# Performance work log

Measured on AMD Instinct MI355X. Metric: run time of the kernel, lower is better.

## Reference

```python
import jax, jax.numpy as jnp
import numpy as np

HEADS = 8
DIM_HEAD = 64
SCALE = DIM_HEAD ** -0.5


def setup_inputs() -> dict:
    key = jax.random.key(0)
    ks = jax.random.split(key, 7)
    B, N, M, D, INNER = 2, 4096, 4096, 1024, HEADS * DIM_HEAD
    x = jax.random.normal(ks[0], (B, N, D), dtype=jnp.float32)
    context = jax.random.normal(ks[1], (B, M, D), dtype=jnp.float32)
    Wq = jax.random.normal(ks[2], (D, INNER), dtype=jnp.float32) * 0.02
    Wk = jax.random.normal(ks[3], (D, INNER), dtype=jnp.float32) * 0.02
    Wv = jax.random.normal(ks[4], (D, INNER), dtype=jnp.float32) * 0.02
    Wo = jax.random.normal(ks[5], (INNER, D), dtype=jnp.float32) * 0.02
    bo = jnp.zeros((D,), dtype=jnp.float32)
    return {"x": x, "context": context, "Wq": Wq, "Wk": Wk, "Wv": Wv, "Wo": Wo, "bo": bo}


def reference(x, context, Wq, Wk, Wv, Wo, bo):
    B, N, _ = x.shape
    M = context.shape[1]
    # projections (no bias, as in to_q/to_k/to_v)
    q = (x @ Wq).reshape(B, N, HEADS, DIM_HEAD)        # b n h d
    k = (context @ Wk).reshape(B, M, HEADS, DIM_HEAD)  # b m h d
    v = (context @ Wv).reshape(B, M, HEADS, DIM_HEAD)
    # scaled dot-product attention (the chunk loop in the original is math-equivalent)
    scores = jnp.einsum('bnhd,bmhd->bhnm', q, k) * SCALE
    attn = jax.nn.softmax(scores, axis=-1)
    out = jnp.einsum('bhnm,bmhd->bnhd', attn, v).reshape(B, N, HEADS * DIM_HEAD)
    # to_out: Linear with bias (dropout p=0.0 -> identity)
    return out @ Wo + bo
```

## Files before the change

### kernel.cpp

```cpp
#include <hip/hip_runtime.h>
#include <hip/hip_bf16.h>

typedef short bf16x8 __attribute__((ext_vector_type(8)));
typedef float f32x4 __attribute__((ext_vector_type(4)));
typedef float f32x16 __attribute__((ext_vector_type(16)));

#define MFMA16(a, b, c) __builtin_amdgcn_mfma_f32_16x16x32_bf16((a), (b), (c), 0, 0, 0)
#define MFMA32(a, b, c) __builtin_amdgcn_mfma_f32_32x32x16_bf16((a), (b), (c), 0, 0, 0)

#if __has_builtin(__builtin_amdgcn_exp2f)
#define EXP2(x) __builtin_amdgcn_exp2f(x)
#else
#define EXP2(x) __expf((x) * 0.6931471805599453f)
#endif

__device__ __forceinline__ ushort f2bf(float f) {
  union { float f; unsigned u; } x; x.f = f;
  unsigned u = x.u;
  return (ushort)((u + 0x7fffu + ((u >> 16) & 1u)) >> 16);
}

__device__ __forceinline__ unsigned cvtpk(float a, float b) {
  unsigned r;
  asm("v_cvt_pk_bf16_f32 %0, %1, %2" : "=v"(r) : "v"(a), "v"(b));
  return r;
}

__device__ __forceinline__ void plswap(unsigned& a, unsigned& b) {
  asm volatile("v_permlane32_swap_b32 %0, %1" : "+v"(a), "+v"(b));
}

__device__ __forceinline__ float bfbits2f(unsigned hw) {
  union { unsigned u; float f; } x; x.u = hw << 16; return x.f;
}

__device__ __forceinline__ void gl2lds16(const ushort* g, ushort* l) {
  typedef const __attribute__((address_space(1))) unsigned int* gp_t;
  typedef __attribute__((address_space(3))) unsigned int* lp_t;
  __builtin_amdgcn_global_load_lds((gp_t)(const void*)g, (lp_t)(void*)l, 16, 0, 0);
}

__global__ void transpose_qkv(const float* __restrict__ Wq, const float* __restrict__ Wk,
                              const float* __restrict__ Wv, ushort* __restrict__ Wqt,
                              ushort* __restrict__ Wkt, ushort* __restrict__ Wvt,
                              float qscale) {
  __shared__ float t[64][65];
  const int z = blockIdx.z;
  const float* src = z == 0 ? Wq : z == 1 ? Wk : Wv;
  ushort* dst = z == 0 ? Wqt : z == 1 ? Wkt : Wvt;
  const float scale = z == 0 ? qscale : 1.0f;
  const int R = 1024, C = 512;
  const int r0 = blockIdx.y * 64, c0 = blockIdx.x * 64;
  const int tid = threadIdx.x;
#pragma unroll
  for (int i = 0; i < 16; i++) {
    int idx = i * 256 + tid; int rr = idx >> 6, cc = idx & 63;
    t[rr][cc] = src[(size_t)(r0 + rr) * C + c0 + cc];
  }
  __syncthreads();
#pragma unroll
  for (int i = 0; i < 16; i++) {
    int idx = i * 256 + tid; int cc = idx >> 6, rr = idx & 63;
    dst[(size_t)(c0 + cc) * R + r0 + rr] = f2bf(t[rr][cc] * scale);
  }
}

__global__ void transpose_cvt64(const float* __restrict__ src, ushort* __restrict__ dst,
                                int R, int C, float scale) {
  __shared__ float t[64][65];
  const int r0 = blockIdx.y * 64, c0 = blockIdx.x * 64;
  const int tid = threadIdx.x;
#pragma unroll
  for (int i = 0; i < 16; i++) {
    int idx = i * 256 + tid; int rr = idx >> 6, cc = idx & 63;
    t[rr][cc] = src[(size_t)(r0 + rr) * C + c0 + cc];
  }
  __syncthreads();
#pragma unroll
  for (int i = 0; i < 16; i++) {
    int idx = i * 256 + tid; int cc = idx >> 6, rr = idx & 63;
    dst[(size_t)(c0 + cc) * R + r0 + rr] = f2bf(t[rr][cc] * scale);
  }
}

template<int OUT, int AF32, int BF32>
__device__ __forceinline__ void gemm_core(ushort* lA, ushort* lB,
                                          const void* __restrict__ Av,
                                          const void* __restrict__ Bv,
                                          void* __restrict__ Cv,
                                          const float* __restrict__ bias,
                                          int N, int K, int row0, int col0) {
  const int tid = threadIdx.x;
  const int lane = tid & 63, wid = tid >> 6;
  const int lr = lane >> 3;
  const int cswz = ((lane & 7) ^ lr) << 3;
  const int clin = (lane & 7) << 3;
  const int wbyte = (clin * 2) ^ (lr << 4);
  const int wm = (wid >> 1) * 64, wn = (wid & 1) * 64;
  const int lo = lane & 15, hi = lane >> 4;

  f32x4 acc[4][4] = {};

  for (int k0 = 0; k0 < K; k0 += 64) {
    if (AF32) {
      const float* A = (const float*)Av;
      float4 v0[4], v1[4];
#pragma unroll
      for (int i = 0; i < 4; i++) {
        const float* p = A + (size_t)(row0 + (i * 4 + wid) * 8 + lr) * K + k0 + clin;
        v0[i] = *(const float4*)p;
        v1[i] = *(const float4*)(p + 4);
      }
#pragma unroll
      for (int i = 0; i < 4; i++) {
        uint4 w;
        w.x = cvtpk(v0[i].x, v0[i].y);
        w.y = cvtpk(v0[i].z, v0[i].w);
        w.z = cvtpk(v1[i].x, v1[i].y);
        w.w = cvtpk(v1[i].z, v1[i].w);
        *(uint4*)((char*)lA + ((i * 4 + wid) * 8 + lr) * 128 + wbyte) = w;
      }
    } else {
      const ushort* A = (const ushort*)Av;
#pragma unroll
      for (int i = 0; i < 4; i++) {
        int g = i * 4 + wid;
        gl2lds16(A + (size_t)(row0 + g * 8 + lr) * K + k0 + cswz, &lA[g * 512]);
      }
    }
    if (BF32) {
      const float* B = (const float*)Bv;
      float4 v0[4], v1[4];
#pragma unroll
      for (int i = 0; i < 4; i++) {
        const float* p = B + (size_t)(col0 + (i * 4 + wid) * 8 + lr) * K + k0 + clin;
        v0[i] = *(const float4*)p;
        v1[i] = *(const float4*)(p + 4);
      }
#pragma unroll
      for (int i = 0; i < 4; i++) {
        uint4 w;
        w.x = cvtpk(v0[i].x, v0[i].y);
        w.y = cvtpk(v0[i].z, v0[i].w);
        w.z = cvtpk(v1[i].x, v1[i].y);
        w.w = cvtpk(v1[i].z, v1[i].w);
        *(uint4*)((char*)lB + ((i * 4 + wid) * 8 + lr) * 128 + wbyte) = w;
      }
    } else {
      const ushort* B = (const ushort*)Bv;
#pragma unroll
      for (int i = 0; i < 4; i++) {
        int g = i * 4 + wid;
        gl2lds16(B + (size_t)(col0 + g * 8 + lr) * K + k0 + cswz, &lB[g * 512]);
      }
    }
    __syncthreads();
#pragma unroll
    for (int kk = 0; kk < 2; kk++) {
      bf16x8 af[4], bfr[4];
      const int kbyte = kk * 64 + hi * 16;
#pragma unroll
      for (int i = 0; i < 4; i++) {
        int r = wm + i * 16 + lo;
        af[i] = *(const bf16x8*)((const char*)lA + r * 128 + (kbyte ^ ((r & 7) << 4)));
        int c = wn + i * 16 + lo;
        bfr[i] = *(const bf16x8*)((const char*)lB + c * 128 + (kbyte ^ ((c & 7) << 4)));
      }
#pragma unroll
      for (int i = 0; i < 4; i++)
#pragma unroll
        for (int j = 0; j < 4; j++)
          acc[i][j] = MFMA16(af[i], bfr[j], acc[i][j]);
    }
    __syncthreads();
  }

#pragma unroll
  for (int i = 0; i < 4; i++)
#pragma unroll
    for (int j = 0; j < 4; j++)
#pragma unroll
      for (int r = 0; r < 4; r++) {
        int row = row0 + wm + i * 16 + hi * 4 + r;
        int col = col0 + wn + j * 16 + lo;
        float v = acc[i][j][r];
        if (OUT == 1)
          ((float*)Cv)[(size_t)row * N + col] = v + (bias ? bias[col] : 0.f);
        else if (OUT == 0)
          ((ushort*)Cv)[(size_t)row * N + col] = f2bf(v);
        else
          ((ushort*)Cv)[((size_t)(col >> 12) * 512 + row) * 4096 + (col & 4095)] = f2bf(v);
      }
}

__global__ __launch_bounds__(256, 3)
void proj_fused(const float* __restrict__ x, const float* __restrict__ ctx,
                const ushort* __restrict__ Wqt, const ushort* __restrict__ Wkt,
                const ushort* __restrict__ Wvt,
                ushort* __restrict__ Qb, ushort* __restrict__ Kb, ushort* __restrict__ Vtb) {
  __shared__ __align__(16) ushort lA[128 * 64];
  __shared__ __align__(16) ushort lB[128 * 64];
  const int bid = blockIdx.x;
  if (bid < 512) {
    const float* A    = bid < 256 ? x   : ctx;
    const ushort* Bt  = bid < 256 ? Wqt : Wkt;
    ushort* C         = bid < 256 ? Qb  : Kb;
    const int l = bid & 255;
    gemm_core<0, 1, 0>(lA, lB, A, Bt, C, nullptr, 512, 1024, (l & 63) * 128, (l >> 6) * 128);
  } else {
    const int l = bid - 512;
    gemm_core<2, 0, 1>(lA, lB, Wvt, ctx, Vtb, nullptr, 8192, 1024, (l & 3) * 128, (l >> 2) * 128);
  }
}

__global__ __launch_bounds__(256, 3)
void out_gemm(const ushort* __restrict__ Ob, const ushort* __restrict__ Wot,
              float* __restrict__ out, const float* __restrict__ bo) {
  __shared__ __align__(16) ushort lA[128 * 64];
  __shared__ __align__(16) ushort lB[128 * 64];
  gemm_core<1, 0, 0>(lA, lB, Ob, Wot, out, bo, 1024, 512, blockIdx.x * 128, blockIdx.y * 128);
}

__global__ __launch_bounds__(256, 4)
void attn_kernel(const ushort* __restrict__ Q, const ushort* __restrict__ Kp,
                 const ushort* __restrict__ Vt, unsigned* __restrict__ Opart,
                 float* __restrict__ Lpart) {
  __shared__ __align__(16) ushort kbuf[2][64 * 64];
  __shared__ __align__(16) ushort vbuf[2][64 * 64];

  const int tid = threadIdx.x;
  const int lane = tid & 63, wid = tid >> 6;
  const int bid = blockIdx.x;
  const int kvh = bid >> 9;
  const int b9 = bid & 511;
  const int bh = (b9 & 7) * 2 + (b9 >> 8);
  const int qblk = (b9 >> 3) & 31;
  const int b = bh >> 3, h = bh & 7;
  const int l31 = lane & 31, hi5 = lane >> 5;
  const int qrow = qblk * 128 + wid * 32 + l31;
  const size_t rowbase = (size_t)b * 4096;
  const int hoff = h * 64;
  const int kv0 = kvh * 1024;
  const int swzk = (l31 & 7) << 4;

  bf16x8 qf[4];
  {
    const ushort* qp = Q + (rowbase + qrow) * 512 + hoff + hi5 * 8;
    qf[0] = *(const bf16x8*)(qp);
    qf[1] = *(const bf16x8*)(qp + 16);
    qf[2] = *(const bf16x8*)(qp + 32);
    qf[3] = *(const bf16x8*)(qp + 48);
  }

  const int r0 = wid * 16 + (lane >> 3);
  const int r1 = r0 + 8;
  const int c00 = ((((lane & 7) * 16) ^ ((r0 & 7) << 4)) >> 1);
  const int c01 = ((((lane & 7) * 16) ^ ((r1 & 7) << 4)) >> 1);
  const ushort* kp0 = Kp + (rowbase + kv0 + r0) * 512 + hoff + c00;
  const ushort* kp1 = Kp + (rowbase + kv0 + r1) * 512 + hoff + c01;
  const ushort* vp0 = Vt + ((size_t)bh * 64 + r0) * 4096 + kv0 + c00;
  const ushort* vp1 = Vt + ((size_t)bh * 64 + r1) * 4096 + kv0 + c01;

  float l_run = 0.f;
  f32x16 o0 = {}, o1 = {};

  gl2lds16(kp0, &kbuf[0][wid * 1024]);
  gl2lds16(kp1, &kbuf[0][wid * 1024 + 512]);
  gl2lds16(vp0, &vbuf[0][wid * 1024]);
  gl2lds16(vp1, &vbuf[0][wid * 1024 + 512]);
  __syncthreads();

  for (int t = 0; t < 16; t++) {
    const int cur = t & 1;
    if (t < 15) {
      const size_t ko = (size_t)(t + 1) * (64 * 512);
      const int vo = (t + 1) * 64;
      gl2lds16(kp0 + ko, &kbuf[cur ^ 1][wid * 1024]);
      gl2lds16(kp1 + ko, &kbuf[cur ^ 1][wid * 1024 + 512]);
      gl2lds16(vp0 + vo, &vbuf[cur ^ 1][wid * 1024]);
      gl2lds16(vp1 + vo, &vbuf[cur ^ 1][wid * 1024 + 512]);
    }
    const char* kb = (const char*)kbuf[cur];
    const char* vb = (const char*)vbuf[cur];

    f32x16 s0 = {}, s1 = {};
    __builtin_amdgcn_s_setprio(1);
#pragma unroll
    for (int kt = 0; kt < 4; kt++) {
      bf16x8 kf = *(const bf16x8*)(kb + l31 * 128 + ((kt * 32 + hi5 * 16) ^ swzk));
      s0 = MFMA32(kf, qf[kt], s0);
    }
#pragma unroll
    for (int kt = 0; kt < 4; kt++) {
      bf16x8 kf = *(const bf16x8*)(kb + (32 + l31) * 128 + ((kt * 32 + hi5 * 16) ^ swzk));
      s1 = MFMA32(kf, qf[kt], s1);
    }
    __builtin_amdgcn_s_setprio(0);

#pragma unroll
    for (int i = 0; i < 16; i++) { s0[i] = EXP2(s0[i]); s1[i] = EXP2(s1[i]); }

    float sm[16];
#pragma unroll
    for (int i = 0; i < 8; i++) sm[i] = s0[2 * i] + s0[2 * i + 1];
#pragma unroll
    for (int i = 0; i < 8; i++) sm[8 + i] = s1[2 * i] + s1[2 * i + 1];
#pragma unroll
    for (int st = 8; st > 0; st >>= 1)
#pragma unroll
      for (int i = 0; i < st; i++) sm[i] = sm[2 * i] + sm[2 * i + 1];
    float rs = sm[0];
    rs += __shfl_xor(rs, 32);
    l_run += rs;

    unsigned p0[8], p1[8];
#pragma unroll
    for (int p = 0; p < 8; p++) {
      p0[p] = cvtpk(s0[2 * p], s0[2 * p + 1]);
      p1[p] = cvtpk(s1[2 * p], s1[2 * p + 1]);
    }
    plswap(p0[0], p0[2]); plswap(p0[1], p0[3]);
    plswap(p0[4], p0[6]); plswap(p0[5], p0[7]);
    plswap(p1[0], p1[2]); plswap(p1[1], p1[3]);
    plswap(p1[4], p1[6]); plswap(p1[5], p1[7]);

    union PF { unsigned u[4]; bf16x8 v; } pf[4];
    pf[0].u[0] = p0[0]; pf[0].u[1] = p0[1]; pf[0].u[2] = p0[2]; pf[0].u[3] = p0[3];
    pf[1].u[0] = p0[4]; pf[1].u[1] = p0[5]; pf[1].u[2] = p0[6]; pf[1].u[3] = p0[7];
    pf[2].u[0] = p1[0]; pf[2].u[1] = p1[1]; pf[2].u[2] = p1[2]; pf[2].u[3] = p1[3];
    pf[3].u[0] = p1[4]; pf[3].u[1] = p1[5]; pf[3].u[2] = p1[6]; pf[3].u[3] = p1[7];

    __builtin_amdgcn_s_setprio(1);
#pragma unroll
    for (int ks = 0; ks < 4; ks++) {
      bf16x8 v0 = *(const bf16x8*)(vb + l31 * 128 + ((ks * 32 + hi5 * 16) ^ swzk));
      bf16x8 v1 = *(const bf16x8*)(vb + (32 + l31) * 128 + ((ks * 32 + hi5 * 16) ^ swzk));
      o0 = MFMA32(v0, pf[ks].v, o0);
      o1 = MFMA32(v1, pf[ks].v, o1);
    }
    __builtin_amdgcn_s_setprio(0);

    __syncthreads();
  }

  const float inv = 1.0f / l_run;
  unsigned* op = Opart + ((size_t)kvh * 65536 + (size_t)bh * 4096 + qrow) * 32;
  {
    uint4 wa, wb;
    wa.x = cvtpk(o0[0] * inv, o0[1] * inv);
    wa.y = cvtpk(o0[2] * inv, o0[3] * inv);
    wa.z = cvtpk(o0[4] * inv, o0[5] * inv);
    wa.w = cvtpk(o0[6] * inv, o0[7] * inv);
    wb.x = cvtpk(o0[8] * inv, o0[9] * inv);
    wb.y = cvtpk(o0[10] * inv, o0[11] * inv);
    wb.z = cvtpk(o0[12] * inv, o0[13] * inv);
    wb.w = cvtpk(o0[14] * inv, o0[15] * inv);
    *(uint4*)(op + hi5 * 8) = wa;
    *(uint4*)(op + hi5 * 8 + 4) = wb;
    wa.x = cvtpk(o1[0] * inv, o1[1] * inv);
    wa.y = cvtpk(o1[2] * inv, o1[3] * inv);
    wa.z = cvtpk(o1[4] * inv, o1[5] * inv);
    wa.w = cvtpk(o1[6] * inv, o1[7] * inv);
    wb.x = cvtpk(o1[8] * inv, o1[9] * inv);
    wb.y = cvtpk(o1[10] * inv, o1[11] * inv);
    wb.z = cvtpk(o1[12] * inv, o1[13] * inv);
    wb.w = cvtpk(o1[14] * inv, o1[15] * inv);
    *(uint4*)(op + 16 + hi5 * 8) = wa;
    *(uint4*)(op + 16 + hi5 * 8 + 4) = wb;
  }
  if (hi5 == 0)
    Lpart[(size_t)kvh * 65536 + (size_t)bh * 4096 + qrow] = l_run;
}

__global__ __launch_bounds__(256)
void attn_merge(const unsigned* __restrict__ Opart, const float* __restrict__ Lpart,
                ushort* __restrict__ Ob) {
  const int idx = blockIdx.x * 256 + threadIdx.x;
  const int qg = idx >> 5, slot = idx & 31;
  float l0 = Lpart[qg];
  float l1 = Lpart[65536 + qg];
  float l2 = Lpart[2 * 65536 + qg];
  float l3 = Lpart[3 * 65536 + qg];
  const float inv = 1.0f / (l0 + l1 + l2 + l3);
  float ra = 0.f, rb = 0.f;
#pragma unroll
  for (int i = 0; i < 4; i++) {
    const float w = (i == 0 ? l0 : i == 1 ? l1 : i == 2 ? l2 : l3) * inv;
    const unsigned u = Opart[((size_t)i * 65536 + qg) * 32 + slot];
    ra += bfbits2f(u & 0xffffu) * w;
    rb += bfbits2f(u >> 16) * w;
  }
  const int dt = slot >> 4, s = slot & 15;
  const int h5 = s >> 3, p = s & 7;
  const int d0 = dt * 32 + 2 * (p & 1) + 8 * (p >> 1) + 4 * h5;
  const int bh = qg >> 12, qrow = qg & 4095;
  unsigned* dst = (unsigned*)(Ob + ((size_t)(bh >> 3) * 4096 + qrow) * 512 + (bh & 7) * 64 + d0);
  *dst = cvtpk(ra, rb);
}

extern "C" void kernel_launch(void* const* d_in, const int* in_sizes, int n_in,
                              void* d_out, int out_size, void* d_ws, size_t ws_size,
                              hipStream_t stream) {
  (void)in_sizes; (void)n_in; (void)out_size;
  const float* x   = (const float*)d_in[0];
  const float* ctx = (const float*)d_in[1];
  const float* Wq  = (const float*)d_in[2];
  const float* Wk  = (const float*)d_in[3];
  const float* Wv  = (const float*)d_in[4];
  const float* Wo  = (const float*)d_in[5];
  const float* bo  = (const float*)d_in[6];

  const float QSCALE = 0.125f * 1.4426950408889634f;
  const size_t MB = 1024 * 1024;
  if (ws_size < 72 * MB) return;
  char* ws = (char*)d_ws;
  ushort* Wqt = (ushort*)(ws + 0 * MB);
  ushort* Wkt = (ushort*)(ws + 1 * MB);
  ushort* Wvt = (ushort*)(ws + 2 * MB);
  ushort* Wot = (ushort*)(ws + 3 * MB);
  unsigned* Opart = (unsigned*)(ws + 4 * MB);
  float*    Lp    = (float*)(ws + 38 * MB);
  ushort* Qb   = (ushort*)(ws + 40 * MB);
  ushort* Kb   = (ushort*)(ws + 48 * MB);
  ushort* Vtb  = (ushort*)(ws + 56 * MB);
  ushort* Ob   = (ushort*)(ws + 64 * MB);

  transpose_qkv<<<dim3(8, 16, 3), dim3(256), 0, stream>>>(Wq, Wk, Wv, Wqt, Wkt, Wvt, QSCALE);
  transpose_cvt64<<<dim3(16, 8), dim3(256), 0, stream>>>(Wo, Wot, 512, 1024, 1.0f);

  proj_fused<<<dim3(768), dim3(256), 0, stream>>>(x, ctx, Wqt, Wkt, Wvt, Qb, Kb, Vtb);

  attn_kernel<<<dim3(2048), dim3(256), 0, stream>>>(Qb, Kb, Vtb, Opart, Lp);
  attn_merge<<<dim3(8192), dim3(256), 0, stream>>>(Opart, Lp, Ob);

  out_gemm<<<dim3(64, 8), dim3(256), 0, stream>>>(Ob, Wot, (float*)d_out, bo);
}
```

Before: 166.2 us.

## Prefetch fp32 GEMM tiles into registers, vectorize epilogue, merge weight transposes

```diff
diff --git a/kernel.cpp b/kernel.cpp
--- a/kernel.cpp
+++ b/kernel.cpp
@@ -40,35 +40,20 @@
   __builtin_amdgcn_global_load_lds((gp_t)(const void*)g, (lp_t)(void*)l, 16, 0, 0);
 }
 
-__global__ void transpose_qkv(const float* __restrict__ Wq, const float* __restrict__ Wk,
-                              const float* __restrict__ Wv, ushort* __restrict__ Wqt,
-                              ushort* __restrict__ Wkt, ushort* __restrict__ Wvt,
+__global__ void transpose_all(const float* __restrict__ Wq, const float* __restrict__ Wk,
+                              const float* __restrict__ Wv, const float* __restrict__ Wo,
+                              ushort* __restrict__ Wqt, ushort* __restrict__ Wkt,
+                              ushort* __restrict__ Wvt, ushort* __restrict__ Wot,
                               float qscale) {
   __shared__ float t[64][65];
   const int z = blockIdx.z;
-  const float* src = z == 0 ? Wq : z == 1 ? Wk : Wv;
-  ushort* dst = z == 0 ? Wqt : z == 1 ? Wkt : Wvt;
-  const float scale = z == 0 ? qscale : 1.0f;
-  const int R = 1024, C = 512;
+  const float* src; ushort* dst; int R, C; float scale = 1.0f;
+  if (z == 0)      { src = Wq; dst = Wqt; R = 1024; C = 512; scale = qscale; }
+  else if (z == 1) { src = Wk; dst = Wkt; R = 1024; C = 512; }
+  else if (z == 2) { src = Wv; dst = Wvt; R = 1024; C = 512; }
+  else             { src = Wo; dst = Wot; R = 512;  C = 1024; }
   const int r0 = blockIdx.y * 64, c0 = blockIdx.x * 64;
-  const int tid = threadIdx.x;
-#pragma unroll
-  for (int i = 0; i < 16; i++) {
-    int idx = i * 256 + tid; int rr = idx >> 6, cc = idx & 63;
-    t[rr][cc] = src[(size_t)(r0 + rr) * C + c0 + cc];
-  }
-  __syncthreads();
-#pragma unroll
-  for (int i = 0; i < 16; i++) {
-    int idx = i * 256 + tid; int cc = idx >> 6, rr = idx & 63;
-    dst[(size_t)(c0 + cc) * R + r0 + rr] = f2bf(t[rr][cc] * scale);
-  }
-}
-
-__global__ void transpose_cvt64(const float* __restrict__ src, ushort* __restrict__ dst,
-                                int R, int C, float scale) {
-  __shared__ float t[64][65];
-  const int r0 = blockIdx.y * 64, c0 = blockIdx.x * 64;
+  if (r0 >= R || c0 >= C) return;
   const int tid = threadIdx.x;
 #pragma unroll
   for (int i = 0; i < 16; i++) {
@@ -99,25 +84,38 @@
   const int wm = (wid >> 1) * 64, wn = (wid & 1) * 64;
   const int lo = lane & 15, hi = lane >> 4;
 
+  const float* Af = (const float*)Av;
+  const float* Bf = (const float*)Bv;
+
+  float4 a0[4], a1[4], b0[4], b1[4];
+  if (AF32) {
+#pragma unroll
+    for (int i = 0; i < 4; i++) {
+      const float* p = Af + (size_t)(row0 + (i * 4 + wid) * 8 + lr) * K + clin;
+      a0[i] = *(const float4*)p;
+      a1[i] = *(const float4*)(p + 4);
+    }
+  }
+  if (BF32) {
+#pragma unroll
+    for (int i = 0; i < 4; i++) {
+      const float* p = Bf + (size_t)(col0 + (i * 4 + wid) * 8 + lr) * K + clin;
+      b0[i] = *(const float4*)p;
+      b1[i] = *(const float4*)(p + 4);
+    }
+  }
+
   f32x4 acc[4][4] = {};
 
   for (int k0 = 0; k0 < K; k0 += 64) {
     if (AF32) {
-      const float* A = (const float*)Av;
-      float4 v0[4], v1[4];
-#pragma unroll
-      for (int i = 0; i < 4; i++) {
-        const float* p = A + (size_t)(row0 + (i * 4 + wid) * 8 + lr) * K + k0 + clin;
-        v0[i] = *(const float4*)p;
-        v1[i] = *(const float4*)(p + 4);
-      }
 #pragma unroll
       for (int i = 0; i < 4; i++) {
         uint4 w;
-        w.x = cvtpk(v0[i].x, v0[i].y);
-        w.y = cvtpk(v0[i].z, v0[i].w);
-        w.z = cvtpk(v1[i].x, v1[i].y);
-        w.w = cvtpk(v1[i].z, v1[i].w);
+        w.x = cvtpk(a0[i].x, a0[i].y);
+        w.y = cvtpk(a0[i].z, a0[i].w);
+        w.z = cvtpk(a1[i].x, a1[i].y);
+        w.w = cvtpk(a1[i].z, a1[i].w);
         *(uint4*)((char*)lA + ((i * 4 + wid) * 8 + lr) * 128 + wbyte) = w;
       }
     } else {
@@ -129,21 +127,13 @@
       }
     }
     if (BF32) {
-      const float* B = (const float*)Bv;
-      float4 v0[4], v1[4];
-#pragma unroll
-      for (int i = 0; i < 4; i++) {
-        const float* p = B + (size_t)(col0 + (i * 4 + wid) * 8 + lr) * K + k0 + clin;
-        v0[i] = *(const float4*)p;
-        v1[i] = *(const float4*)(p + 4);
-      }
 #pragma unroll
       for (int i = 0; i < 4; i++) {
         uint4 w;
-        w.x = cvtpk(v0[i].x, v0[i].y);
-        w.y = cvtpk(v0[i].z, v0[i].w);
-        w.z = cvtpk(v1[i].x, v1[i].y);
-        w.w = cvtpk(v1[i].z, v1[i].w);
+        w.x = cvtpk(b0[i].x, b0[i].y);
+        w.y = cvtpk(b0[i].z, b0[i].w);
+        w.z = cvtpk(b1[i].x, b1[i].y);
+        w.w = cvtpk(b1[i].z, b1[i].w);
         *(uint4*)((char*)lB + ((i * 4 + wid) * 8 + lr) * 128 + wbyte) = w;
       }
     } else {
@@ -155,6 +145,24 @@
       }
     }
     __syncthreads();
+
+    if (AF32 && k0 + 64 < K) {
+#pragma unroll
+      for (int i = 0; i < 4; i++) {
+        const float* p = Af + (size_t)(row0 + (i * 4 + wid) * 8 + lr) * K + (k0 + 64) + clin;
+        a0[i] = *(const float4*)p;
+        a1[i] = *(const float4*)(p + 4);
+      }
+    }
+    if (BF32 && k0 + 64 < K) {
+#pragma unroll
+      for (int i = 0; i < 4; i++) {
+        const float* p = Bf + (size_t)(col0 + (i * 4 + wid) * 8 + lr) * K + (k0 + 64) + clin;
+        b0[i] = *(const float4*)p;
+        b1[i] = *(const float4*)(p + 4);
+      }
+    }
+
 #pragma unroll
     for (int kk = 0; kk < 2; kk++) {
       bf16x8 af[4], bfr[4];
@@ -170,7 +178,7 @@
       for (int i = 0; i < 4; i++)
 #pragma unroll
         for (int j = 0; j < 4; j++)
-          acc[i][j] = MFMA16(af[i], bfr[j], acc[i][j]);
+          acc[i][j] = MFMA16(bfr[j], af[i], acc[i][j]);
     }
     __syncthreads();
   }
@@ -178,19 +186,23 @@
 #pragma unroll
   for (int i = 0; i < 4; i++)
 #pragma unroll
-    for (int j = 0; j < 4; j++)
-#pragma unroll
-      for (int r = 0; r < 4; r++) {
-        int row = row0 + wm + i * 16 + hi * 4 + r;
-        int col = col0 + wn + j * 16 + lo;
-        float v = acc[i][j][r];
-        if (OUT == 1)
-          ((float*)Cv)[(size_t)row * N + col] = v + (bias ? bias[col] : 0.f);
-        else if (OUT == 0)
-          ((ushort*)Cv)[(size_t)row * N + col] = f2bf(v);
-        else
-          ((ushort*)Cv)[((size_t)(col >> 12) * 512 + row) * 4096 + (col & 4095)] = f2bf(v);
-      }
+    for (int j = 0; j < 4; j++) {
+      const int row = row0 + wm + i * 16 + lo;
+      const int col = col0 + wn + j * 16 + hi * 4;
+      const f32x4 v = acc[i][j];
+      if (OUT == 1) {
+        const float4 bv = *(const float4*)(bias + col);
+        float4 w;
+        w.x = v[0] + bv.x; w.y = v[1] + bv.y; w.z = v[2] + bv.z; w.w = v[3] + bv.w;
+        *(float4*)((float*)Cv + (size_t)row * N + col) = w;
+      } else if (OUT == 0) {
+        uint2 w; w.x = cvtpk(v[0], v[1]); w.y = cvtpk(v[2], v[3]);
+        *(uint2*)((ushort*)Cv + (size_t)row * N + col) = w;
+      } else {
+        uint2 w; w.x = cvtpk(v[0], v[1]); w.y = cvtpk(v[2], v[3]);
+        *(uint2*)((ushort*)Cv + ((size_t)(col >> 12) * 512 + row) * 4096 + (col & 4095)) = w;
+      }
+    }
 }
 
 __global__ __launch_bounds__(256, 3)
@@ -425,8 +437,8 @@
   ushort* Vtb  = (ushort*)(ws + 56 * MB);
   ushort* Ob   = (ushort*)(ws + 64 * MB);
 
-  transpose_qkv<<<dim3(8, 16, 3), dim3(256), 0, stream>>>(Wq, Wk, Wv, Wqt, Wkt, Wvt, QSCALE);
-  transpose_cvt64<<<dim3(16, 8), dim3(256), 0, stream>>>(Wo, Wot, 512, 1024, 1.0f);
+  transpose_all<<<dim3(16, 16, 4), dim3(256), 0, stream>>>(Wq, Wk, Wv, Wo,
+                                                           Wqt, Wkt, Wvt, Wot, QSCALE);
 
   proj_fused<<<dim3(768), dim3(256), 0, stream>>>(x, ctx, Wqt, Wkt, Wvt, Qb, Kb, Vtb);
 
```

Measured after the change: 157.4 us. 1.06x faster.
